# Kernel optimization log

Measured on AMD Instinct MI355X. Metric: run time of the kernel, lower is better.

## Reference

```python
import jax, jax.numpy as jnp
import numpy as np

B, T, C, H = 512, 4096, 7, 3  # batch, time, 7 classes, 3 heads


def setup_inputs() -> dict:
    key = jax.random.key(0)
    k0, k1, k2, k3, k4, k5 = jax.random.split(key, 6)
    # outputs are treated as probabilities (log is taken directly); keep them in (0.01, 1]
    mk_out = lambda k: jax.random.uniform(k, (B, T, C), dtype=jnp.float32, minval=0.01, maxval=1.0)
    return {
        "out0": mk_out(k0),
        "out1": mk_out(k1),
        "out2": mk_out(k2),
        "labels_3": jax.random.randint(k3, (B, T, H), 0, C, dtype=jnp.int64),
        "mask": jax.random.uniform(k4, (B, T), dtype=jnp.float32),
        "reward": jax.random.uniform(k5, (B, T, H), dtype=jnp.float32),
    }


def reference(out0, out1, out2, labels_3, mask, reward):
    N = B * T
    outs = jnp.stack([out0, out1, out2], axis=0).reshape(H, N, C)   # [3, N, 7]
    labels = labels_3.reshape(N, H).T                               # [3, N]
    rw = reward.reshape(N, H).T                                     # [3, N]
    valid = mask.reshape(N) < 0.5                                   # [N] bool
    n_valid = valid.sum()

    # gather probability of the true class per head: op[h, n] = outs[h, n, labels[h, n]]
    op = jnp.take_along_axis(outs, labels[:, :, None], axis=2)[..., 0]  # [3, N]
    # original: sum_h -dot(log(op_h), sr_h) / n_valid  (n_valid identical across heads)
    loss = -jnp.where(valid[None, :], jnp.log(op) * rw, 0.0).sum() / n_valid

    pred = jnp.argmax(outs, axis=-1)                                # [3, N]
    correct = jnp.all(pred == labels, axis=0) & valid               # product over heads on valid positions
    n_correct = correct.sum()
    return loss, n_correct, n_valid
```

## Files before the change

kernel.cpp:

```cpp
#include <hip/hip_runtime.h>

constexpr long long N_ROWS = 512LL * 4096LL;
constexpr int BLOCK = 256;
constexpr int RPT   = 4;
constexpr int NBLOCKS = (int)(N_ROWS / ((long long)BLOCK * RPT));

__global__ __launch_bounds__(BLOCK, 4) void shortloss_main(
    const float* __restrict__ out0,
    const float* __restrict__ out1,
    const float* __restrict__ out2,
    const int*   __restrict__ labels,
    const float* __restrict__ mask,
    const float* __restrict__ reward,
    float4*      __restrict__ partials)
{
    const int tid = threadIdx.x;
    const long long g = (long long)blockIdx.x * BLOCK + tid;

    const float* outs[3] = {out0, out1, out2};

    float4 mkv = ((const float4*)mask)[g];
    const float mk[4] = {mkv.x, mkv.y, mkv.z, mkv.w};

    int lb[12];
    {
        const int4* lp = (const int4*)labels;
        #pragma unroll
        for (int j = 0; j < 3; ++j) {
            int4 t = lp[3 * g + j];
            lb[4*j+0] = t.x; lb[4*j+1] = t.y; lb[4*j+2] = t.z; lb[4*j+3] = t.w;
        }
    }
    float rw[12];
    {
        const float4* rp = (const float4*)reward;
        #pragma unroll
        for (int j = 0; j < 3; ++j) {
            float4 t = rp[3 * g + j];
            rw[4*j+0] = t.x; rw[4*j+1] = t.y; rw[4*j+2] = t.z; rw[4*j+3] = t.w;
        }
    }

    float lsum[4] = {0.f, 0.f, 0.f, 0.f};
    int   ok[4]   = {1, 1, 1, 1};
    #pragma unroll
    for (int h = 0; h < 3; ++h) {
        float o[28];
        const float4* op = (const float4*)outs[h];
        #pragma unroll
        for (int j = 0; j < 7; ++j) {
            float4 t = op[7 * g + j];
            o[4*j+0] = t.x; o[4*j+1] = t.y; o[4*j+2] = t.z; o[4*j+3] = t.w;
        }
        #pragma unroll
        for (int i = 0; i < 4; ++i) {
            const int lbl = lb[3*i + h];
            const float* v = o + 7*i;

            float best = v[0]; int bestc = 0;
            #pragma unroll
            for (int cc = 1; cc < 7; ++cc)
                if (v[cc] > best) { best = v[cc]; bestc = cc; }

            float opv = v[0];
            #pragma unroll
            for (int cc = 1; cc < 7; ++cc)
                opv = (lbl == cc) ? v[cc] : opv;

            lsum[i] += __logf(opv) * rw[3*i + h];
            ok[i]   &= (bestc == lbl) ? 1 : 0;
        }
    }

    float L = 0.0f;
    int   C = 0, V = 0;
    #pragma unroll
    for (int i = 0; i < 4; ++i) {
        const bool valid = mk[i] < 0.5f;
        V += valid ? 1 : 0;
        L += valid ? lsum[i] : 0.0f;
        C += (valid && ok[i]) ? 1 : 0;
    }

    #pragma unroll
    for (int off = 32; off > 0; off >>= 1) {
        L += __shfl_down(L, off, 64);
        C += __shfl_down(C, off, 64);
        V += __shfl_down(V, off, 64);
    }
    __shared__ float sL[BLOCK / 64];
    __shared__ int   sC[BLOCK / 64], sV[BLOCK / 64];
    const int wave = tid >> 6;
    if ((tid & 63) == 0) { sL[wave] = L; sC[wave] = C; sV[wave] = V; }
    __syncthreads();
    if (tid == 0) {
        float l = 0.0f; int cc = 0, vv = 0;
        #pragma unroll
        for (int w = 0; w < BLOCK / 64; ++w) { l += sL[w]; cc += sC[w]; vv += sV[w]; }
        partials[blockIdx.x] = make_float4(l, (float)cc, (float)vv, 0.0f);
    }
}

__global__ __launch_bounds__(256) void shortloss_reduce(
    const float4* __restrict__ partials,
    float* __restrict__ out)
{
    float L = 0.0f, C = 0.0f, V = 0.0f;
    for (int i = threadIdx.x; i < NBLOCKS; i += 256) {
        float4 p = partials[i];
        L += p.x; C += p.y; V += p.z;
    }
    #pragma unroll
    for (int off = 32; off > 0; off >>= 1) {
        L += __shfl_down(L, off, 64);
        C += __shfl_down(C, off, 64);
        V += __shfl_down(V, off, 64);
    }
    __shared__ float sL[4], sC[4], sV[4];
    const int wave = threadIdx.x >> 6;
    if ((threadIdx.x & 63) == 0) { sL[wave] = L; sC[wave] = C; sV[wave] = V; }
    __syncthreads();
    if (threadIdx.x == 0) {
        float l = 0.0f, c = 0.0f, v = 0.0f;
        #pragma unroll
        for (int w = 0; w < 4; ++w) { l += sL[w]; c += sC[w]; v += sV[w]; }
        out[0] = -l / v;
        out[1] = c;
        out[2] = v;
    }
}

extern "C" void kernel_launch(void* const* d_in, const int* in_sizes, int n_in,
                              void* d_out, int out_size, void* d_ws, size_t ws_size,
                              hipStream_t stream) {
    const float* out0   = (const float*)d_in[0];
    const float* out1   = (const float*)d_in[1];
    const float* out2   = (const float*)d_in[2];
    const int*   labels = (const int*)  d_in[3];
    const float* mask   = (const float*)d_in[4];
    const float* reward = (const float*)d_in[5];

    float4* partials = (float4*)d_ws;

    shortloss_main<<<NBLOCKS, BLOCK, 0, stream>>>(
        out0, out1, out2, labels, mask, reward, partials);
    shortloss_reduce<<<1, 256, 0, stream>>>(partials, (float*)d_out);
}
```

Measured before the change: 227.6 us.

## Double-buffer class probabilities into LDS with async global loads per wave

Each block becomes a single 64-thread wave that processes four chunks of 256 rows. For each chunk, the three probability tensors are copied into one of two LDS buffers using coalesced global_load_lds instructions. Manual vmcnt waits let the next chunk's load overlap the current chunk's compute, and the cross-wave shared-memory reduction is removed. The cost is about 43KB of LDS per one-wave block, which sharply limits waves per CU. Correctness also depends on the hand-written wait counts matching the exact number of loads issued.

```diff
diff --git a/kernel.cpp b/kernel.cpp
--- a/kernel.cpp
+++ b/kernel.cpp
@@ -1,11 +1,21 @@
 #include <hip/hip_runtime.h>
 
 constexpr long long N_ROWS = 512LL * 4096LL;
-constexpr int BLOCK = 256;
-constexpr int RPT   = 4;
-constexpr int NBLOCKS = (int)(N_ROWS / ((long long)BLOCK * RPT));
+constexpr int BLOCK      = 64;
+constexpr int CHUNK_ROWS = 256;
+constexpr int CPB        = 4;
+constexpr int NBLOCKS    = (int)(N_ROWS / ((long long)CHUNK_ROWS * CPB));
 
-__global__ __launch_bounds__(BLOCK, 4) void shortloss_main(
+constexpr int BUFW = 5376;
+
+__device__ __forceinline__ void async16(const float* g, float* l) {
+    __builtin_amdgcn_global_load_lds(
+        (const __attribute__((address_space(1))) unsigned int*)g,
+        (__attribute__((address_space(3))) unsigned int*)l,
+        16, 0, 0);
+}
+
+__global__ __launch_bounds__(BLOCK) void shortloss_main(
     const float* __restrict__ out0,
     const float* __restrict__ out1,
     const float* __restrict__ out2,
@@ -14,73 +24,103 @@
     const float* __restrict__ reward,
     float4*      __restrict__ partials)
 {
+    __shared__ float lds0[BUFW];
+    __shared__ float lds1[BUFW];
     const int tid = threadIdx.x;
-    const long long g = (long long)blockIdx.x * BLOCK + tid;
-
+    const int c0  = blockIdx.x * CPB;
     const float* outs[3] = {out0, out1, out2};
 
-    float4 mkv = ((const float4*)mask)[g];
-    const float mk[4] = {mkv.x, mkv.y, mkv.z, mkv.w};
+    auto stage = [&](int c, float* buf) {
+        #pragma unroll
+        for (int h = 0; h < 3; ++h) {
+            const float* src = outs[h] + (size_t)c * 1792;
+            float*       dst = buf + h * 1792;
+            #pragma unroll
+            for (int j = 0; j < 7; ++j)
+                async16(src + j * 256 + 4 * (size_t)tid, dst + j * 256 + 4 * tid);
+        }
+    };
 
-    int lb[12];
-    {
-        const int4* lp = (const int4*)labels;
+    auto side = [&](int c, int* lb, float* rw, float* mk) {
+        const long long g = (long long)c * 64 + tid;
+        const int4*   lp = (const int4*)labels;
+        const float4* rp = (const float4*)reward;
         #pragma unroll
         for (int j = 0; j < 3; ++j) {
             int4 t = lp[3 * g + j];
             lb[4*j+0] = t.x; lb[4*j+1] = t.y; lb[4*j+2] = t.z; lb[4*j+3] = t.w;
+            float4 u = rp[3 * g + j];
+            rw[4*j+0] = u.x; rw[4*j+1] = u.y; rw[4*j+2] = u.z; rw[4*j+3] = u.w;
         }
-    }
-    float rw[12];
-    {
-        const float4* rp = (const float4*)reward;
+        float4 m = ((const float4*)mask)[g];
+        mk[0] = m.x; mk[1] = m.y; mk[2] = m.z; mk[3] = m.w;
+    };
+
+    float L = 0.0f;
+    int   C = 0, V = 0;
+
+    auto compute = [&](const float* buf, const int* lb, const float* rw, const float* mk) {
+        float lsum[4] = {0.f, 0.f, 0.f, 0.f};
+        int   ok[4]   = {1, 1, 1, 1};
         #pragma unroll
-        for (int j = 0; j < 3; ++j) {
-            float4 t = rp[3 * g + j];
-            rw[4*j+0] = t.x; rw[4*j+1] = t.y; rw[4*j+2] = t.z; rw[4*j+3] = t.w;
-        }
-    }
+        for (int h = 0; h < 3; ++h) {
+            float o[28];
+            const float4* bp = (const float4*)(buf + h * 1792) + 7 * tid;
+            #pragma unroll
+            for (int j = 0; j < 7; ++j) {
+                float4 t = bp[j];
+                o[4*j+0] = t.x; o[4*j+1] = t.y; o[4*j+2] = t.z; o[4*j+3] = t.w;
+            }
+            #pragma unroll
+            for (int i = 0; i < 4; ++i) {
+                const int lbl = lb[3*i + h];
+                const float* v = o + 7*i;
 
-    float lsum[4] = {0.f, 0.f, 0.f, 0.f};
-    int   ok[4]   = {1, 1, 1, 1};
-    #pragma unroll
-    for (int h = 0; h < 3; ++h) {
-        float o[28];
-        const float4* op = (const float4*)outs[h];
-        #pragma unroll
-        for (int j = 0; j < 7; ++j) {
-            float4 t = op[7 * g + j];
-            o[4*j+0] = t.x; o[4*j+1] = t.y; o[4*j+2] = t.z; o[4*j+3] = t.w;
+                float best = v[0]; int bestc = 0;
+                #pragma unroll
+                for (int cc = 1; cc < 7; ++cc)
+                    if (v[cc] > best) { best = v[cc]; bestc = cc; }
+
+                float opv = v[0];
+                #pragma unroll
+                for (int cc = 1; cc < 7; ++cc)
+                    opv = (lbl == cc) ? v[cc] : opv;
+
+                lsum[i] += __logf(opv) * rw[3*i + h];
+                ok[i]   &= (bestc == lbl) ? 1 : 0;
+            }
         }
         #pragma unroll
         for (int i = 0; i < 4; ++i) {
-            const int lbl = lb[3*i + h];
-            const float* v = o + 7*i;
+            const bool valid = mk[i] < 0.5f;
+            V += valid ? 1 : 0;
+            L += valid ? lsum[i] : 0.0f;
+            C += (valid && ok[i]) ? 1 : 0;
+        }
+    };
 
-            float best = v[0]; int bestc = 0;
-            #pragma unroll
-            for (int cc = 1; cc < 7; ++cc)
-                if (v[cc] > best) { best = v[cc]; bestc = cc; }
+    int   lbA[12], lbB[12];
+    float rwA[12], rwB[12], mkA[4], mkB[4];
 
-            float opv = v[0];
-            #pragma unroll
-            for (int cc = 1; cc < 7; ++cc)
-                opv = (lbl == cc) ? v[cc] : opv;
+    stage(c0 + 0, lds0);
+    side (c0 + 0, lbA, rwA, mkA);
+    stage(c0 + 1, lds1);
+    asm volatile("s_waitcnt vmcnt(21)" ::: "memory");
+    compute(lds0, lbA, rwA, mkA);
 
-            lsum[i] += __logf(opv) * rw[3*i + h];
-            ok[i]   &= (bestc == lbl) ? 1 : 0;
-        }
-    }
+    side (c0 + 1, lbB, rwB, mkB);
+    stage(c0 + 2, lds0);
+    asm volatile("s_waitcnt vmcnt(21)" ::: "memory");
+    compute(lds1, lbB, rwB, mkB);
 
-    float L = 0.0f;
-    int   C = 0, V = 0;
-    #pragma unroll
-    for (int i = 0; i < 4; ++i) {
-        const bool valid = mk[i] < 0.5f;
-        V += valid ? 1 : 0;
-        L += valid ? lsum[i] : 0.0f;
-        C += (valid && ok[i]) ? 1 : 0;
-    }
+    side (c0 + 2, lbA, rwA, mkA);
+    stage(c0 + 3, lds1);
+    asm volatile("s_waitcnt vmcnt(21)" ::: "memory");
+    compute(lds0, lbA, rwA, mkA);
+
+    side (c0 + 3, lbB, rwB, mkB);
+    asm volatile("s_waitcnt vmcnt(7)" ::: "memory");
+    compute(lds1, lbB, rwB, mkB);
 
     #pragma unroll
     for (int off = 32; off > 0; off >>= 1) {
@@ -88,17 +128,8 @@
         C += __shfl_down(C, off, 64);
         V += __shfl_down(V, off, 64);
     }
-    __shared__ float sL[BLOCK / 64];
-    __shared__ int   sC[BLOCK / 64], sV[BLOCK / 64];
-    const int wave = tid >> 6;
-    if ((tid & 63) == 0) { sL[wave] = L; sC[wave] = C; sV[wave] = V; }
-    __syncthreads();
-    if (tid == 0) {
-        float l = 0.0f; int cc = 0, vv = 0;
-        #pragma unroll
-        for (int w = 0; w < BLOCK / 64; ++w) { l += sL[w]; cc += sC[w]; vv += sV[w]; }
-        partials[blockIdx.x] = make_float4(l, (float)cc, (float)vv, 0.0f);
-    }
+    if (tid == 0)
+        partials[blockIdx.x] = make_float4(L, (float)C, (float)V, 0.0f);
 }
 
 __global__ __launch_bounds__(256) void shortloss_reduce(
```

Result: no change. 231.5 us (+1.7%).
